# Kernel optimization log

Measured on AMD Instinct MI355X. Metric: run time of the kernel, lower is better.

Reference implementation:

```python
import jax, jax.numpy as jnp
import numpy as np

C = 512
K = 3
DIL = 1
EPS = 1e-6


def weight_quant(w):
    # BitNet b1.58 ternary quantization with straight-through estimator:
    # scale = mean(|w|); w_q = clamp(round(w/scale), -1, 1) * scale
    s = jnp.maximum(jnp.mean(jnp.abs(w)), 1e-5)
    q = jnp.clip(jnp.round(w / s), -1.0, 1.0) * s
    return w + jax.lax.stop_gradient(q - w)


def conv1d(x, w, b, padding, dilation):
    # x: [B, C, L], w: [O, I, K]
    y = jax.lax.conv_general_dilated(
        x, w, window_strides=(1,), padding=[(padding, padding)],
        rhs_dilation=(dilation,), dimension_numbers=("NCH", "OIH", "NCH"))
    return y + b[None, :, None]


def setup_inputs() -> dict:
    key = jax.random.key(0)
    k0, k1, k2, k3, k4 = jax.random.split(key, 5)
    fan_in = C * K
    lim = 1.0 / np.sqrt(fan_in)
    x = jax.random.normal(k0, (16, C, 4096), dtype=jnp.float32)
    w1 = jax.random.uniform(k1, (C, C, K), jnp.float32, -lim, lim)
    b1 = jax.random.uniform(k2, (C,), jnp.float32, -lim, lim)
    w2 = jax.random.uniform(k3, (C, C, K), jnp.float32, -lim, lim)
    b2 = jax.random.uniform(k4, (C,), jnp.float32, -lim, lim)
    g = jnp.ones((C,), dtype=jnp.float32)  # RMSNorm gain
    return {"x": x, "w1": w1, "b1": b1, "w2": w2, "b2": b2, "g": g}


def reference(x, w1, b1, w2, b2, g):
    residual = x
    # RMSNorm over channel axis (original transposes to [B,L,C], norms last dim)
    ms = jnp.mean(jnp.square(x), axis=1, keepdims=True)
    h = x * jax.lax.rsqrt(ms + EPS) * g[None, :, None]
    h = jax.nn.silu(h)
    p1 = (K * DIL - DIL) // 2
    h = conv1d(h, weight_quant(w1), b1, p1, DIL)
    h = jax.nn.silu(h)
    h = conv1d(h, weight_quant(w2), b2, K // 2, 1)
    return h + residual
```

## Files before the change

### kernel.cpp

```cpp
#include <hip/hip_runtime.h>

#define BATCH 16
#define CCH 512
#define LEN 4096
#define LPAD 4098

typedef unsigned short u16;
typedef __bf16 bf16x8 __attribute__((ext_vector_type(8)));
typedef float f32x4 __attribute__((ext_vector_type(4)));
typedef u16 u16x8 __attribute__((ext_vector_type(8)));
typedef u16 u16x4 __attribute__((ext_vector_type(4)));

__device__ __forceinline__ u16 f2bf(float f) {
    unsigned u = __float_as_uint(f);
    u = (u + 0x7fffu + ((u >> 16) & 1u)) >> 16;
    return (u16)u;
}
__device__ __forceinline__ float bf2f(u16 v) {
    return __uint_as_float(((unsigned)v) << 16);
}
__device__ __forceinline__ float silu_f(float v) {
    return v / (1.f + __expf(-v));
}
__device__ __forceinline__ void async16(const u16* g, u16* l) {
    __builtin_amdgcn_global_load_lds(
        (const __attribute__((address_space(1))) unsigned int*)g,
        (__attribute__((address_space(3))) unsigned int*)l, 16, 0, 0);
}

#define SBAR() __builtin_amdgcn_sched_barrier(0)
#define HWBAR() { SBAR(); __builtin_amdgcn_s_barrier(); SBAR(); }
#define WAIT_LGKM0() { asm volatile("s_waitcnt lgkmcnt(0)" ::: "memory"); SBAR(); }
#define WAIT_VM(n) { asm volatile("s_waitcnt vmcnt(" #n ")" ::: "memory"); SBAR(); }

__global__ __launch_bounds__(256)
void absmean_partial(const float* __restrict__ w1, const float* __restrict__ w2,
                     float* __restrict__ part) {
    const int tid = threadIdx.x;
    const int base = blockIdx.x * 3072;
    float s1 = 0.f, s2 = 0.f;
    for (int i = tid; i < 3072; i += 256) {
        s1 += fabsf(w1[base + i]);
        s2 += fabsf(w2[base + i]);
    }
    __shared__ float r1[256], r2[256];
    r1[tid] = s1; r2[tid] = s2;
    __syncthreads();
    for (int off = 128; off > 0; off >>= 1) {
        if (tid < off) { r1[tid] += r1[tid + off]; r2[tid] += r2[tid + off]; }
        __syncthreads();
    }
    if (tid == 0) { part[blockIdx.x] = r1[0]; part[256 + blockIdx.x] = r2[0]; }
}

__global__ __launch_bounds__(256)
void finalize_scale(const float* __restrict__ part, float* __restrict__ sv) {
    const int tid = threadIdx.x;
    __shared__ float r1[256], r2[256];
    r1[tid] = part[tid]; r2[tid] = part[256 + tid];
    __syncthreads();
    for (int off = 128; off > 0; off >>= 1) {
        if (tid < off) { r1[tid] += r1[tid + off]; r2[tid] += r2[tid + off]; }
        __syncthreads();
    }
    if (tid == 0) {
        sv[0] = fmaxf(r1[0] * (1.f / 786432.f), 1e-5f);
        sv[1] = fmaxf(r2[0] * (1.f / 786432.f), 1e-5f);
    }
}

__global__ __launch_bounds__(256)
void quantize_w(const float* __restrict__ w, const float* __restrict__ sv,
                int sidx, u16* __restrict__ wqt) {
    const int idx = blockIdx.x * 256 + threadIdx.x;
    const float s = sv[sidx];
    float q = rintf(w[idx] / s);
    q = fmaxf(-1.f, fminf(1.f, q));
    const int o   = idx / 1536;
    const int rem = idx - o * 1536;
    const int i   = rem / 3;
    const int k   = rem - i * 3;
    wqt[k * (CCH * CCH) + o * CCH + i] = f2bf(q);
}

__global__ __launch_bounds__(256)
void zero_pads(u16* __restrict__ h, u16* __restrict__ h1) {
    const int idx = blockIdx.x * 256 + threadIdx.x;
    const int b = idx >> 10;
    const int r = (idx >> 9) & 1;
    const int i = idx & 511;
    const size_t off = ((size_t)b * LPAD + (r ? (LPAD - 1) : 0)) * CCH + i;
    h[off] = 0;
    h1[off] = 0;
}

__global__ __launch_bounds__(256)
void rms_silu_transpose(const float* __restrict__ x, const float* __restrict__ g,
                        u16* __restrict__ h_t) {
    __shared__ u16   xt[CCH][33];
    __shared__ float red[8][32];
    __shared__ float rinv[32];
    const int tid = threadIdx.x;
    const int bb  = blockIdx.x >> 7;
    const int l0  = (blockIdx.x & 127) << 5;

    const size_t xbase = (size_t)bb * CCH * LEN + l0;
    {
        const int i_hi = tid >> 3;
        const int l4   = (tid & 7) << 2;
        #pragma unroll
        for (int it = 0; it < 16; ++it) {
            const int i = it * 32 + i_hi;
            const float4 v = *(const float4*)&x[xbase + (size_t)i * LEN + l4];
            xt[i][l4 + 0] = f2bf(v.x);
            xt[i][l4 + 1] = f2bf(v.y);
            xt[i][l4 + 2] = f2bf(v.z);
            xt[i][l4 + 3] = f2bf(v.w);
        }
    }
    __syncthreads();
    {
        const int l = tid & 31, seg = tid >> 5;
        const int ibeg = seg * 64;
        float ss = 0.f;
        #pragma unroll 8
        for (int i = ibeg; i < ibeg + 64; ++i) {
            const float v = bf2f(xt[i][l]);
            ss += v * v;
        }
        red[seg][l] = ss;
    }
    __syncthreads();
    if (tid < 32) {
        float tot = 0.f;
        #pragma unroll
        for (int k2 = 0; k2 < 8; ++k2) tot += red[k2][tid];
        rinv[tid] = rsqrtf(tot * (1.f / 512.f) + 1e-6f);
    }
    __syncthreads();
    {
        const int l  = tid >> 3;
        const int i0 = (tid & 7) << 6;
        const float ri = rinv[l];
        const size_t ob = ((size_t)bb * LPAD + l0 + l + 1) * CCH + i0;
        for (int ii = 0; ii < 64; ii += 8) {
            u16x8 ov;
            #pragma unroll
            for (int jj = 0; jj < 8; ++jj) {
                const int i = i0 + ii + jj;
                float v = bf2f(xt[i][l]) * ri * g[i];
                ov[jj] = f2bf(silu_f(v));
            }
            *(u16x8*)&h_t[ob + ii] = ov;
        }
    }
}

template<int EPI>
__global__ __launch_bounds__(512)
void conv_gemm8(const u16* __restrict__ Bsrc, const u16* __restrict__ Wq,
                const float* __restrict__ sptr, const float* __restrict__ bias,
                const float* __restrict__ resid, u16* __restrict__ outb,
                float* __restrict__ outf) {
    extern __shared__ u16 lds[];
    const int tid  = threadIdx.x;
    const int lane = tid & 63;
    const int wave = tid >> 6;
    const int wm = wave >> 2;
    const int wn = wave & 3;

    const int wgid = (blockIdx.x & 7) * 64 + (blockIdx.x >> 3);
    const int mt = wgid & 1;
    const int nt = wgid >> 1;
    const int o0 = mt << 8;
    const int bb = nt >> 4;
    const int l0 = (nt & 15) << 8;

    const int sr  = tid >> 3;
    const int scu = ((tid & 7) << 3) ^ ((sr & 7) << 3);
    const int sdst = tid << 3;

    const u16* aSrcBase = Wq + (size_t)o0 * CCH + scu;
    const u16* bSrcBase = Bsrc + ((size_t)bb * LPAD + l0) * CCH + scu;

    auto stage = [&](int pb, int T, int h, int ks2, int i02) {
        #pragma unroll
        for (int j = 0; j < 2; ++j) {
            const int r = h * 128 + j * 64 + sr;
            const u16* src = (T == 0)
                ? aSrcBase + ks2 * (CCH * CCH) + r * CCH + i02
                : bSrcBase + (size_t)(r + ks2) * CCH + i02;
            async16(src, &lds[pb * 32768 + T * 16384 + h * 8192 + j * 4096 + sdst]);
        }
    };

    const int swz = (lane & 7) << 3;
    const int c0 = ((lane >> 4) << 3) ^ swz;
    const int c1 = (((lane >> 4) << 3) + 32) ^ swz;
    const int aB = wm * 8192 + (lane & 15) * 64;
    const int bB = 16384 + (wn >> 1) * 8192 + ((wn & 1) * 64 + (lane & 15)) * 64;

    bf16x8 ar[4][2], br[4][2];
    f32x4 acc[8][4];
    #pragma unroll
    for (int m = 0; m < 8; ++m)
        #pragma unroll
        for (int n = 0; n < 4; ++n)
            acc[m][n] = (f32x4){0.f, 0.f, 0.f, 0.f};

    auto rdA = [&](int cbuf, int mh) {
        #pragma unroll
        for (int mm = 0; mm < 4; ++mm) {
            const int base = cbuf * 32768 + aB + (mh * 4 + mm) * 1024;
            ar[mm][0] = *(const bf16x8*)&lds[base + c0];
            ar[mm][1] = *(const bf16x8*)&lds[base + c1];
        }
    };
    auto rdB = [&](int cbuf, int nh) {
        #pragma unroll
        for (int nn = 0; nn < 2; ++nn) {
            const int fn = nh * 2 + nn;
            const int base = cbuf * 32768 + bB + fn * 1024;
            br[fn][0] = *(const bf16x8*)&lds[base + c0];
            br[fn][1] = *(const bf16x8*)&lds[base + c1];
        }
    };
    auto mfma16 = [&](int mh, int nh) {
        __builtin_amdgcn_s_setprio(1);
        #pragma unroll
        for (int kk = 0; kk < 2; ++kk)
            #pragma unroll
            for (int mm = 0; mm < 4; ++mm)
                #pragma unroll
                for (int nn = 0; nn < 2; ++nn)
                    acc[mh * 4 + mm][nh * 2 + nn] =
                        __builtin_amdgcn_mfma_f32_16x16x32_bf16(
                            ar[mm][kk], br[nh * 2 + nn][kk],
                            acc[mh * 4 + mm][nh * 2 + nn], 0, 0, 0);
        __builtin_amdgcn_s_setprio(0);
    };

    stage(0, 0, 0, 0, 0);
    stage(0, 0, 1, 0, 0);
    stage(0, 1, 0, 0, 0);
    stage(0, 1, 1, 0, 0);
    stage(1, 1, 0, 0, 64);
    stage(1, 1, 1, 0, 64);
    WAIT_VM(4);
    HWBAR();

    auto iterbody = [&](int j, bool full) {
        const int tO  = 2 * j + 1;
        const int tE2 = 2 * j + 2;
        const int tO2 = 2 * j + 3;
        const int ksO = tO >> 3,  iO  = (tO & 7) << 6;
        const int ksE = tE2 >> 3, iE  = (tE2 & 7) << 6;
        const int ksP = tO2 >> 3, iP  = (tO2 & 7) << 6;
        rdA(0, 0); rdB(0, 0);
        stage(1, 0, 0, ksO, iO);
        HWBAR(); WAIT_LGKM0(); mfma16(0, 0); HWBAR();
        rdB(0, 1);
        stage(1, 0, 1, ksO, iO);
        HWBAR(); WAIT_LGKM0(); mfma16(0, 1); HWBAR();
        rdA(0, 1);
        if (full) stage(0, 1, 0, ksE, iE);
        HWBAR(); WAIT_LGKM0(); mfma16(1, 1); HWBAR();
        if (full) stage(0, 1, 1, ksE, iE);
        HWBAR(); mfma16(1, 0);
        if (full) { WAIT_VM(4); } else { WAIT_VM(0); }
        HWBAR();
        rdA(1, 0); rdB(1, 0);
        if (full) stage(0, 0, 0, ksE, iE);
        HWBAR(); WAIT_LGKM0(); mfma16(0, 0); HWBAR();
        rdB(1, 1);
        if (full) stage(0, 0, 1, ksE, iE);
        HWBAR(); WAIT_LGKM0(); mfma16(0, 1); HWBAR();
        rdA(1, 1);
        if (full) stage(1, 1, 0, ksP, iP);
        HWBAR(); WAIT_LGKM0(); mfma16(1, 1); HWBAR();
        if (full) stage(1, 1, 1, ksP, iP);
        HWBAR(); mfma16(1, 0);
        if (full) { WAIT_VM(4); }
        HWBAR();
    };

    for (int j = 0; j < 11; ++j) iterbody(j, true);
    iterbody(11, false);

    const float sc = sptr[0];

    if (EPI == 1) {
        #pragma unroll
        for (int m = 0; m < 8; ++m) {
            const int o_loc = wm * 128 + m * 16 + ((lane >> 4) << 2);
            const int ob = o0 + o_loc;
            const float b0 = bias[ob + 0], b1 = bias[ob + 1];
            const float b2 = bias[ob + 2], b3 = bias[ob + 3];
            #pragma unroll
            for (int n = 0; n < 4; ++n) {
                const int l_loc = wn * 64 + n * 16 + (lane & 15);
                const f32x4 a = acc[m][n];
                u16x4 ov;
                ov[0] = f2bf(silu_f(sc * a[0] + b0));
                ov[1] = f2bf(silu_f(sc * a[1] + b1));
                ov[2] = f2bf(silu_f(sc * a[2] + b2));
                ov[3] = f2bf(silu_f(sc * a[3] + b3));
                char* p = (char*)lds + l_loc * 512 +
                          (((unsigned)(o_loc << 1)) ^ ((l_loc & 7) << 4));
                *(u16x4*)p = ov;
            }
        }
        __syncthreads();
        const int l_r = tid >> 2;
        const int oq  = (tid & 3) << 3;
        #pragma unroll
        for (int pass = 0; pass < 2; ++pass) {
            const int lr = l_r + pass * 128;
            u16* gdst = outb + ((size_t)bb * LPAD + l0 + lr + 1) * CCH + o0 + oq;
            char* srp = (char*)lds + lr * 512;
            const int swz2 = (lr & 7) << 4;
            #pragma unroll
            for (int c = 0; c < 8; ++c) {
                const uint4 v = *(const uint4*)(srp + (((oq << 1) + c * 64) ^ swz2));
                *(uint4*)(gdst + c * 32) = v;
            }
        }
    } else {
        const int lbase = l0 + wn * 64 + (lane & 15);
        const int obase = o0 + wm * 128 + ((lane >> 4) << 2);
        #pragma unroll
        for (int m = 0; m < 8; ++m) {
            const int ob = obase + m * 16;
            #pragma unroll
            for (int n = 0; n < 4; ++n) {
                const int l = lbase + n * 16;
                const f32x4 a = acc[m][n];
                #pragma unroll
                for (int jj = 0; jj < 4; ++jj) {
                    const size_t idx = ((size_t)bb * CCH + (ob + jj)) * LEN + l;
                    outf[idx] = sc * a[jj] + bias[ob + jj] + resid[idx];
                }
            }
        }
    }
}

extern "C" void kernel_launch(void* const* d_in, const int* in_sizes, int n_in,
                              void* d_out, int out_size, void* d_ws, size_t ws_size,
                              hipStream_t stream) {
    const float* x  = (const float*)d_in[0];
    const float* w1 = (const float*)d_in[1];
    const float* b1 = (const float*)d_in[2];
    const float* w2 = (const float*)d_in[3];
    const float* b2 = (const float*)d_in[4];
    const float* g  = (const float*)d_in[5];
    float* out = (float*)d_out;

    char* ws = (char*)d_ws;
    float* sv   = (float*)ws;
    float* part = (float*)(ws + 256);
    u16* wq1   = (u16*)(ws + 4096);
    u16* wq2   = (u16*)(ws + 4096 + 1572864);
    u16* h_t   = (u16*)(ws + 4096 + 2 * 1572864);
    u16* h1_t  = (u16*)(ws + 4096 + 2 * 1572864 + 67141632);

    hipFuncSetAttribute((const void*)conv_gemm8<1>,
                        hipFuncAttributeMaxDynamicSharedMemorySize, 131072);
    hipFuncSetAttribute((const void*)conv_gemm8<2>,
                        hipFuncAttributeMaxDynamicSharedMemorySize, 131072);

    absmean_partial<<<dim3(256), dim3(256), 0, stream>>>(w1, w2, part);
    finalize_scale<<<dim3(1), dim3(256), 0, stream>>>(part, sv);
    quantize_w<<<dim3(3072), dim3(256), 0, stream>>>(w1, sv, 0, wq1);
    quantize_w<<<dim3(3072), dim3(256), 0, stream>>>(w2, sv, 1, wq2);
    zero_pads<<<dim3(64), dim3(256), 0, stream>>>(h_t, h1_t);
    rms_silu_transpose<<<dim3(2048), dim3(256), 0, stream>>>(x, g, h_t);
    conv_gemm8<1><<<dim3(512), dim3(512), 131072, stream>>>(h_t, wq1, sv, b1,
                                                            nullptr, h1_t, nullptr);
    conv_gemm8<2><<<dim3(512), dim3(512), 131072, stream>>>(h1_t, wq2, sv + 1, b2,
                                                            x, nullptr, out);
}
```

Measured before the change: 322.1 us.

## Replace interleaved ping-pong K-loop with simple whole-tile double buffering

Replaces the hand-interleaved main loop with a plain double-buffered loop over the 24 K tiles. The old loop staged A and B halves between MFMA groups and used partial vmcnt waits. The new loop prefetches the whole next tile into the other buffer, runs all four MFMA quadrants, then waits for all outstanding memory operations and takes one barrier. It also changes the tile order so the three kernel taps are the inner index instead of the channel chunks, which may change L2 reuse. The aim is fewer barriers and simpler scheduling, at the risk of less fine-grained overlap between loads and MFMA.

```diff
diff --git a/kernel.cpp b/kernel.cpp
--- a/kernel.cpp
+++ b/kernel.cpp
@@ -193,6 +193,12 @@
             async16(src, &lds[pb * 32768 + T * 16384 + h * 8192 + j * 4096 + sdst]);
         }
     };
+    auto stage_full = [&](int pb, int ks2, int i02) {
+        stage(pb, 0, 0, ks2, i02);
+        stage(pb, 0, 1, ks2, i02);
+        stage(pb, 1, 0, ks2, i02);
+        stage(pb, 1, 1, ks2, i02);
+    };
 
     const int swz = (lane & 7) << 3;
     const int c0 = ((lane >> 4) << 3) ^ swz;
@@ -240,52 +246,25 @@
         __builtin_amdgcn_s_setprio(0);
     };
 
-    stage(0, 0, 0, 0, 0);
-    stage(0, 0, 1, 0, 0);
-    stage(0, 1, 0, 0, 0);
-    stage(0, 1, 1, 0, 0);
-    stage(1, 1, 0, 0, 64);
-    stage(1, 1, 1, 0, 64);
-    WAIT_VM(4);
+    stage_full(0, 0, 0);
+    WAIT_VM(0);
     HWBAR();
 
-    auto iterbody = [&](int j, bool full) {
-        const int tO  = 2 * j + 1;
-        const int tE2 = 2 * j + 2;
-        const int tO2 = 2 * j + 3;
-        const int ksO = tO >> 3,  iO  = (tO & 7) << 6;
-        const int ksE = tE2 >> 3, iE  = (tE2 & 7) << 6;
-        const int ksP = tO2 >> 3, iP  = (tO2 & 7) << 6;
-        rdA(0, 0); rdB(0, 0);
-        stage(1, 0, 0, ksO, iO);
-        HWBAR(); WAIT_LGKM0(); mfma16(0, 0); HWBAR();
-        rdB(0, 1);
-        stage(1, 0, 1, ksO, iO);
-        HWBAR(); WAIT_LGKM0(); mfma16(0, 1); HWBAR();
-        rdA(0, 1);
-        if (full) stage(0, 1, 0, ksE, iE);
-        HWBAR(); WAIT_LGKM0(); mfma16(1, 1); HWBAR();
-        if (full) stage(0, 1, 1, ksE, iE);
-        HWBAR(); mfma16(1, 0);
-        if (full) { WAIT_VM(4); } else { WAIT_VM(0); }
+    for (int t = 0; t < 24; ++t) {
+        const int cur = t & 1;
+        if (t + 1 < 24) {
+            const int tn = t + 1;
+            stage_full(cur ^ 1, tn % 3, (tn / 3) << 6);
+        }
+        rdB(cur, 0); rdB(cur, 1);
+        rdA(cur, 0);
+        mfma16(0, 0); mfma16(0, 1);
+        rdA(cur, 1);
+        mfma16(1, 1); mfma16(1, 0);
+        WAIT_LGKM0();
+        WAIT_VM(0);
         HWBAR();
-        rdA(1, 0); rdB(1, 0);
-        if (full) stage(0, 0, 0, ksE, iE);
-        HWBAR(); WAIT_LGKM0(); mfma16(0, 0); HWBAR();
-        rdB(1, 1);
-        if (full) stage(0, 0, 1, ksE, iE);
-        HWBAR(); WAIT_LGKM0(); mfma16(0, 1); HWBAR();
-        rdA(1, 1);
-        if (full) stage(1, 1, 0, ksP, iP);
-        HWBAR(); WAIT_LGKM0(); mfma16(1, 1); HWBAR();
-        if (full) stage(1, 1, 1, ksP, iP);
-        HWBAR(); mfma16(1, 0);
-        if (full) { WAIT_VM(4); }
-        HWBAR();
-    };
-
-    for (int j = 0; j < 11; ++j) iterbody(j, true);
-    iterbody(11, false);
+    }
 
     const float sc = sptr[0];
 
```

After: 314.5 us. 1.02x faster.
